# Performance work log

Hardware: AMD Instinct MI355X
Metric: run time of the kernel (lower is better)

The kernel has to match this reference:

```python
import jax, jax.numpy as jnp
import numpy as np

B, S, D = 4, 2048, 1024
H = 16
HD = D // H
PF = 4096
EPS = 1e-5


def setup_inputs() -> dict:
    key = jax.random.key(0)
    ks = jax.random.split(key, 16)
    s = 1.0 / np.sqrt(D)
    inp = {
        'src': jax.random.normal(ks[0], (B, S, D), jnp.float32),
        'Wq': jax.random.normal(ks[1], (D, D), jnp.float32) * s,
        'bq': jnp.zeros((D,), jnp.float32),
        'Wk': jax.random.normal(ks[2], (D, D), jnp.float32) * s,
        'bk': jnp.zeros((D,), jnp.float32),
        'Wv': jax.random.normal(ks[3], (D, D), jnp.float32) * s,
        'bv': jnp.zeros((D,), jnp.float32),
        'Wo': jax.random.normal(ks[4], (D, D), jnp.float32) * s,
        'bo': jnp.zeros((D,), jnp.float32),
        'g1': jnp.ones((D,), jnp.float32),
        'b1': jnp.zeros((D,), jnp.float32),
        'W1': jax.random.normal(ks[5], (D, PF), jnp.float32) * s,
        'bf1': jnp.zeros((PF,), jnp.float32),
        'W2': jax.random.normal(ks[6], (PF, D), jnp.float32) * (1.0 / np.sqrt(PF)),
        'bf2': jnp.zeros((D,), jnp.float32),
        'g2': jnp.ones((D,), jnp.float32),
        'b2': jnp.zeros((D,), jnp.float32),
    }
    return inp


def _layer_norm(x, g, b):
    mu = jnp.mean(x, axis=-1, keepdims=True)
    var = jnp.mean(jnp.square(x - mu), axis=-1, keepdims=True)
    return (x - mu) * jax.lax.rsqrt(var + EPS) * g + b


def reference(src, Wq, bq, Wk, bk, Wv, bv, Wo, bo, g1, b1, W1, bf1, W2, bf2, g2, b2):
    scale = 1.0 / np.sqrt(HD)
    # QKV projections -> [B, H, S, HD]
    q = (src @ Wq + bq).reshape(B, S, H, HD).transpose(0, 2, 1, 3)
    k = (src @ Wk + bk).reshape(B, S, H, HD).transpose(0, 2, 1, 3)
    v = (src @ Wv + bv).reshape(B, S, H, HD).transpose(0, 2, 1, 3)
    # attention scores [B, H, S, S]
    attn = jax.nn.softmax(jnp.einsum('bhqd,bhkd->bhqk', q, k) * scale, axis=-1)
    x = jnp.einsum('bhqk,bhkd->bhqd', attn, v)
    x = x.transpose(0, 2, 1, 3).reshape(B, S, D)
    attn_out = x @ Wo + bo
    # residual + LN (dropout is identity at p=0)
    src1 = _layer_norm(src + attn_out, g1, b1)
    # positionwise FFN: Linear -> Dropout -> ReLU -> Linear
    ff = jax.nn.relu(src1 @ W1 + bf1) @ W2 + bf2
    return _layer_norm(src1 + ff, g2, b2)
```

## Files before the change

### kernel.cpp

```cpp
#include <hip/hip_runtime.h>

#define BB 4
#define SS 2048
#define DD 1024
#define HH 16
#define PFF 4096
#define MR 8192

typedef unsigned short u16;
typedef __attribute__((ext_vector_type(8))) short s16x8;
typedef __attribute__((ext_vector_type(4))) float f32x4v;
typedef __attribute__((ext_vector_type(16))) float f32x16;
typedef __attribute__((ext_vector_type(4))) unsigned short u16x4;
typedef __attribute__((ext_vector_type(8))) unsigned short u16x8;

__device__ inline u16 f2bf(float f) {
  union { float f; unsigned u; } v; v.f = f;
  unsigned r = v.u + 0x7FFFu + ((v.u >> 16) & 1u);
  return (u16)(r >> 16);
}

__device__ inline float bf2f(u16 x) {
  union { unsigned u; float f; } v;
  v.u = ((unsigned)x) << 16;
  return v.f;
}

__device__ inline unsigned cvtpk_bf16(float lo, float hi) {
  unsigned r;
  asm("v_cvt_pk_bf16_f32 %0, %1, %2" : "=v"(r) : "v"(lo), "v"(hi));
  return r;
}

__device__ inline void gload16(const void* g, void* l) {
  __builtin_amdgcn_global_load_lds(
      (const __attribute__((address_space(1))) void*)g,
      (__attribute__((address_space(3))) void*)l, 16, 0, 0);
}

__device__ inline f32x4v MFMA(s16x8 a, s16x8 b, f32x4v c) {
  return __builtin_amdgcn_mfma_f32_16x16x32_bf16(a, b, c, 0, 0, 0);
}
__device__ inline f32x16 MFMA32(s16x8 a, s16x8 b, f32x16 c) {
  return __builtin_amdgcn_mfma_f32_32x32x16_bf16(a, b, c, 0, 0, 0);
}

#define RAWBAR()                          \
  do {                                    \
    asm volatile("" ::: "memory");        \
    __builtin_amdgcn_s_barrier();         \
    asm volatile("" ::: "memory");        \
  } while (0)
#define WAITVM(N) asm volatile("s_waitcnt vmcnt(" #N ")" ::: "memory")

__device__ inline s16x8 ldfrag(const u16* base, int row, int colByte) {
  return *(const s16x8*)((const char*)base + row * 128 + (colByte ^ ((row & 7) << 4)));
}

template <int RELU, int OUTBF, int SCQ, int VT>
__global__ __launch_bounds__(512, 1) void gemm256(
    const u16* __restrict__ A, const u16* __restrict__ Bt,
    const float* __restrict__ bias, float* __restrict__ Cf,
    u16* __restrict__ Cb, u16* __restrict__ Vt, int M, int N, int K,
    int ntx) {
  constexpr int BUF = 16384;
  __shared__ __align__(128) u16 lds[3 * BUF];
  const int t = threadIdx.x;
  const int lane = t & 63, w = t >> 6;
  const int wr = w >> 2, wc = w & 3;
  const int g = lane >> 4, q = lane & 15;

  const int cpx = gridDim.x >> 3;
  const int wg = (blockIdx.x & 7) * cpx + (blockIdx.x >> 3);
  const int row0 = (wg / ntx) * 256, col0 = (wg % ntx) * 256;

  f32x4v acc[8][4];
#pragma unroll
  for (int m = 0; m < 8; ++m)
#pragma unroll
    for (int n = 0; n < 4; ++n) acc[m][n] = (f32x4v){0.f, 0.f, 0.f, 0.f};

  const int sr0 = t >> 2, sc0 = (t & 3) * 8;
  const u16* Ag0 = A + (size_t)(row0 + sr0) * K + sc0;
  const u16* Ag1 = A + (size_t)(row0 + sr0 + 128) * K + sc0;
  const u16* Bg0 = Bt + (size_t)(col0 + sr0) * K + sc0;
  const u16* Bg1 = Bt + (size_t)(col0 + sr0 + 128) * K + sc0;
  const int wud = (t & ~63) * 8;

#define STAGE_A(kt, buf)                                          \
  do {                                                            \
    u16* ab_ = &lds[(buf) * BUF];                                 \
    gload16(Ag0 + (kt) * 32, ab_ + wud);                          \
    gload16(Ag1 + (kt) * 32, ab_ + 4096 + wud);                   \
  } while (0)
#define STAGE_B(kt, buf)                                          \
  do {                                                            \
    u16* bb_ = &lds[(buf) * BUF + 8192];                          \
    gload16(Bg0 + (kt) * 32, bb_ + wud);                          \
    gload16(Bg1 + (kt) * 32, bb_ + 4096 + wud);                   \
  } while (0)

  const int NT = K / 32;
  STAGE_A(0, 0); STAGE_B(0, 0);
  STAGE_A(1, 1); STAGE_B(1, 1);
  WAITVM(4);
  RAWBAR();

  int cur = 0, nxt = 2;
  for (int kt = 0; kt < NT; ++kt) {
    const u16* ab = &lds[cur * BUF];
    const u16* bb = ab + 8192;
    const bool pf = (kt + 2 < NT);
    if (pf) STAGE_A(kt + 2, nxt);
    s16x8 bf_[4], af_[4];
#pragma unroll
    for (int n = 0; n < 4; ++n)
      bf_[n] = *(const s16x8*)&bb[(wc * 64 + n * 16 + q) * 32 + g * 8];
#pragma unroll
    for (int m = 0; m < 4; ++m)
      af_[m] = *(const s16x8*)&ab[(wr * 128 + m * 16 + q) * 32 + g * 8];
    RAWBAR();
    __builtin_amdgcn_s_setprio(1);
#pragma unroll
    for (int m = 0; m < 4; ++m)
#pragma unroll
      for (int n = 0; n < 4; ++n) acc[m][n] = MFMA(af_[m], bf_[n], acc[m][n]);
    __builtin_amdgcn_s_setprio(0);
    RAWBAR();
    if (pf) STAGE_B(kt + 2, nxt);
#pragma unroll
    for (int m = 0; m < 4; ++m)
      af_[m] = *(const s16x8*)&ab[(wr * 128 + (m + 4) * 16 + q) * 32 + g * 8];
    RAWBAR();
    __builtin_amdgcn_s_setprio(1);
#pragma unroll
    for (int m = 0; m < 4; ++m)
#pragma unroll
      for (int n = 0; n < 4; ++n)
        acc[m + 4][n] = MFMA(af_[m], bf_[n], acc[m + 4][n]);
    __builtin_amdgcn_s_setprio(0);
    if (kt + 1 < NT) {
      if (pf) WAITVM(4);
      else WAITVM(0);
    }
    RAWBAR();
    cur = (cur == 2) ? 0 : cur + 1;
    nxt = (nxt == 2) ? 0 : nxt + 1;
  }
#undef STAGE_A
#undef STAGE_B

#pragma unroll
  for (int n = 0; n < 4; ++n) {
    const int col = col0 + wc * 64 + 16 * n + q;
    const float bv = bias ? bias[col] : 0.f;
#pragma unroll
    for (int m = 0; m < 8; ++m) {
      const int row = row0 + wr * 128 + 16 * m + 4 * g;
      if (VT && col >= 2048) {
        const int hd = col - 2048;
        u16x4 o;
#pragma unroll
        for (int r = 0; r < 4; ++r) o[r] = f2bf(acc[m][n][r] + bv);
        *(u16x4*)&Vt[((size_t)((row >> 11) * 16 + (hd >> 6)) * 64 +
                      (hd & 63)) * SS + (row & 2047)] = o;
      } else {
#pragma unroll
        for (int r = 0; r < 4; ++r) {
          float v = acc[m][n][r] + bv;
          if (RELU) v = fmaxf(v, 0.f);
          if (SCQ && col < DD) v *= 0.18033688011112042f;
          if (OUTBF) Cb[(size_t)(row + r) * N + col] = f2bf(v);
          else Cf[(size_t)(row + r) * N + col] = v;
        }
      }
    }
  }
}

template <int RELU>
__global__ __launch_bounds__(256, 3) void gemm128(
    const u16* __restrict__ A, const u16* __restrict__ Bt,
    const float* __restrict__ bias, float* __restrict__ Cf,
    int M, int N, int K, int ntx) {
  constexpr int BUF = 8192;
  __shared__ __align__(128) u16 lds[3 * BUF];
  const int t = threadIdx.x;
  const int lane = t & 63, w = t >> 6;
  const int wr = w >> 1, wc = w & 1;
  const int g = lane >> 4, q = lane & 15;

  const int cpx = gridDim.x >> 3;
  const int wg = (blockIdx.x & 7) * cpx + (blockIdx.x >> 3);
  const int row0 = (wg / ntx) * 128, col0 = (wg % ntx) * 128;

  f32x4v acc[4][4];
#pragma unroll
  for (int m = 0; m < 4; ++m)
#pragma unroll
    for (int n = 0; n < 4; ++n) acc[m][n] = (f32x4v){0.f, 0.f, 0.f, 0.f};

  const int sr0 = t >> 2, sc0 = (t & 3) * 8;
  const u16* Ag0 = A + (size_t)(row0 + sr0) * K + sc0;
  const u16* Ag1 = A + (size_t)(row0 + sr0 + 64) * K + sc0;
  const u16* Bg0 = Bt + (size_t)(col0 + sr0) * K + sc0;
  const u16* Bg1 = Bt + (size_t)(col0 + sr0 + 64) * K + sc0;
  const int wud = (t & ~63) * 8;

#define STAGE_A(kt, buf)                                          \
  do {                                                            \
    u16* ab_ = &lds[(buf) * BUF];                                 \
    gload16(Ag0 + (kt) * 32, ab_ + wud);                          \
    gload16(Ag1 + (kt) * 32, ab_ + 2048 + wud);                   \
  } while (0)
#define STAGE_B(kt, buf)                                          \
  do {                                                            \
    u16* bb_ = &lds[(buf) * BUF + 4096];                          \
    gload16(Bg0 + (kt) * 32, bb_ + wud);                          \
    gload16(Bg1 + (kt) * 32, bb_ + 2048 + wud);                   \
  } while (0)

  const int NT = K / 32;
  STAGE_A(0, 0); STAGE_B(0, 0);
  STAGE_A(1, 1); STAGE_B(1, 1);
  WAITVM(4);
  RAWBAR();

  int cur = 0, nxt = 2;
  for (int kt = 0; kt < NT; ++kt) {
    const u16* ab = &lds[cur * BUF];
    const u16* bb = ab + 4096;
    const bool pf = (kt + 2 < NT);
    if (pf) STAGE_A(kt + 2, nxt);
    s16x8 bf_[4], af_[2];
#pragma unroll
    for (int n = 0; n < 4; ++n)
      bf_[n] = *(const s16x8*)&bb[(wc * 64 + n * 16 + q) * 32 + g * 8];
#pragma unroll
    for (int m = 0; m < 2; ++m)
      af_[m] = *(const s16x8*)&ab[(wr * 64 + m * 16 + q) * 32 + g * 8];
    RAWBAR();
    __builtin_amdgcn_s_setprio(1);
#pragma unroll
    for (int m = 0; m < 2; ++m)
#pragma unroll
      for (int n = 0; n < 4; ++n) acc[m][n] = MFMA(af_[m], bf_[n], acc[m][n]);
    __builtin_amdgcn_s_setprio(0);
    RAWBAR();
    if (pf) STAGE_B(kt + 2, nxt);
#pragma unroll
    for (int m = 0; m < 2; ++m)
      af_[m] = *(const s16x8*)&ab[(wr * 64 + (m + 2) * 16 + q) * 32 + g * 8];
    RAWBAR();
    __builtin_amdgcn_s_setprio(1);
#pragma unroll
    for (int m = 0; m < 2; ++m)
#pragma unroll
      for (int n = 0; n < 4; ++n)
        acc[m + 2][n] = MFMA(af_[m], bf_[n], acc[m + 2][n]);
    __builtin_amdgcn_s_setprio(0);
    if (kt + 1 < NT) {
      if (pf) WAITVM(4);
      else WAITVM(0);
    }
    RAWBAR();
    cur = (cur == 2) ? 0 : cur + 1;
    nxt = (nxt == 2) ? 0 : nxt + 1;
  }
#undef STAGE_A
#undef STAGE_B

#pragma unroll
  for (int n = 0; n < 4; ++n) {
    const int col = col0 + wc * 64 + 16 * n + q;
    const float bv = bias ? bias[col] : 0.f;
#pragma unroll
    for (int m = 0; m < 4; ++m) {
      const int row = row0 + wr * 64 + 16 * m + 4 * g;
#pragma unroll
      for (int r = 0; r < 4; ++r) {
        float v = acc[m][n][r] + bv;
        if (RELU) v = fmaxf(v, 0.f);
        Cf[(size_t)(row + r) * N + col] = v;
      }
    }
  }
}

__global__ __launch_bounds__(256, 4) void attn_mfma(
    const u16* __restrict__ qkv, const u16* __restrict__ vt,
    u16* __restrict__ xb) {
  __shared__ __align__(128) u16 lds[16384];

  const int t = threadIdx.x;
  const int w = t >> 6, lane = t & 63;
  const int q = lane & 31, hi = lane >> 5;
  const int qg = w >> 1;
  const int kg = w & 1;

  const int flat = blockIdx.x;
  const int xcd = flat & 7;
  const int j = flat >> 3;
  const int bh = xcd * 8 + (j & 7);
  const int qb = j >> 3;
  const int b = bh >> 4, h = bh & 15;
  const int q0 = qb * 64;
  const int qcol = h * 64, kcol = DD + h * 64;

  const int r0 = t >> 3;
  const int sc = ((t & 7) ^ (r0 & 7)) * 8;
  const int ldst = (t & ~63) * 16;

  const u16* ks0 = qkv + (size_t)(b * SS + r0) * 3072 + kcol + sc;
  const u16* ks1 = ks0 + (size_t)32 * 3072;
  const u16* vs0 = vt + (size_t)(bh * 64 + r0) * SS + sc;
  const u16* vs1 = vs0 + (size_t)32 * SS;

  {
    const u16* Qsrc = qkv + (size_t)(b * SS + q0 + r0) * 3072 + qcol + sc;
    gload16(Qsrc, (char*)lds + ldst);
    gload16(Qsrc + (size_t)32 * 3072, (char*)lds + 4096 + ldst);
  }
  WAITVM(0);
  RAWBAR();
  s16x8 qf[4];
  {
    const u16* Qw = lds + qg * 2048;
#pragma unroll
    for (int s = 0; s < 4; ++s) qf[s] = ldfrag(Qw, q, 32 * s + 16 * hi);
  }
  asm volatile("s_waitcnt lgkmcnt(0)" ::: "memory");
  __builtin_amdgcn_sched_barrier(0);
  RAWBAR();

#define STAGE(B)                                              \
  do {                                                        \
    gload16(ks0, (char*)lds + (B) + ldst);                    \
    gload16(ks1, (char*)lds + (B) + 4096 + ldst);             \
    gload16(vs0, (char*)lds + (B) + 8192 + ldst);             \
    gload16(vs1, (char*)lds + (B) + 12288 + ldst);            \
    ks0 += (size_t)64 * 3072; ks1 += (size_t)64 * 3072;       \
    vs0 += 64; vs1 += 64;                                     \
  } while (0)

  s16x8 onesv;
#pragma unroll
  for (int i = 0; i < 8; ++i) onesv[i] = (short)0x3F80;

  f32x16 zf;
#pragma unroll
  for (int i = 0; i < 16; ++i) zf[i] = 0.f;

  f32x16 oac0, oac1, lacc;
#pragma unroll
  for (int i = 0; i < 16; ++i) { oac0[i] = 0.f; oac1[i] = 0.f; lacc[i] = 0.f; }

  auto compute = [&](const int B) {
    const u16* Kc = lds + B / 2;
    const u16* Vc = Kc + 4096;

    __builtin_amdgcn_s_setprio(1);
    s16x8 k0 = ldfrag(Kc, kg * 32 + q, 16 * hi);
    f32x16 sa = MFMA32(k0, qf[0], zf);
#pragma unroll
    for (int s = 1; s < 4; ++s) {
      s16x8 ks = ldfrag(Kc, kg * 32 + q, 32 * s + 16 * hi);
      sa = MFMA32(ks, qf[s], sa);
    }
    __builtin_amdgcn_s_setprio(0);

#pragma unroll
    for (int i = 0; i < 16; ++i) sa[i] = exp2f(sa[i]);

    __builtin_amdgcn_s_setprio(1);
#pragma unroll
    for (int sp = 0; sp < 2; ++sp) {
      const int rb = 8 * sp;
      unsigned x0 = cvtpk_bf16(sa[rb + 0], sa[rb + 1]);
      unsigned x1 = cvtpk_bf16(sa[rb + 2], sa[rb + 3]);
      unsigned y0 = cvtpk_bf16(sa[rb + 4], sa[rb + 5]);
      unsigned y1 = cvtpk_bf16(sa[rb + 6], sa[rb + 7]);
      asm("v_permlane32_swap_b32 %0, %1" : "+v"(x0), "+v"(y0));
      asm("v_permlane32_swap_b32 %0, %1" : "+v"(x1), "+v"(y1));
      union { unsigned u[4]; s16x8 v; } pfv;
      pfv.u[0] = x0; pfv.u[1] = x1; pfv.u[2] = y0; pfv.u[3] = y1;
      s16x8 v0 = ldfrag(Vc, q, kg * 64 + 32 * sp + 16 * hi);
      s16x8 v1 = ldfrag(Vc, 32 + q, kg * 64 + 32 * sp + 16 * hi);
      oac0 = MFMA32(v0, pfv.v, oac0);
      oac1 = MFMA32(v1, pfv.v, oac1);
      lacc = MFMA32(onesv, pfv.v, lacc);
    }
    __builtin_amdgcn_s_setprio(0);
  };

  STAGE(0);
  WAITVM(0);
  RAWBAR();
  for (int i = 0; i < 15; ++i) {
    STAGE(16384);
    compute(0);
    WAITVM(0);
    RAWBAR();
    STAGE(0);
    compute(16384);
    WAITVM(0);
    RAWBAR();
  }
  STAGE(16384);
  compute(0);
  WAITVM(0);
  RAWBAR();
  compute(16384);
#undef STAGE

  __syncthreads();
  float* red = (float*)lds;
  if (kg == 1) {
    float* myr = red + (qg * 64 + lane) * 33;
#pragma unroll
    for (int i = 0; i < 16; ++i) { myr[i] = oac0[i]; myr[16 + i] = oac1[i]; }
    myr[32] = lacc[0];
  }
  __syncthreads();
  if (kg == 0) {
    const float* pr = red + (qg * 64 + lane) * 33;
#pragma unroll
    for (int i = 0; i < 16; ++i) { oac0[i] += pr[i]; oac1[i] += pr[16 + i]; }
    const float inv = 1.f / (lacc[0] + pr[32]);
    const size_t row = (size_t)(b * SS + q0 + qg * 32 + q);
    u16* orow = xb + row * DD + qcol;
#pragma unroll
    for (int rr = 0; rr < 4; ++rr) {
      uint2 pw0, pw1;
      pw0.x = cvtpk_bf16(oac0[4 * rr] * inv, oac0[4 * rr + 1] * inv);
      pw0.y = cvtpk_bf16(oac0[4 * rr + 2] * inv, oac0[4 * rr + 3] * inv);
      pw1.x = cvtpk_bf16(oac1[4 * rr] * inv, oac1[4 * rr + 1] * inv);
      pw1.y = cvtpk_bf16(oac1[4 * rr + 2] * inv, oac1[4 * rr + 3] * inv);
      *(uint2*)(orow + 8 * rr + 4 * hi) = pw0;
      *(uint2*)(orow + 32 + 8 * rr + 4 * hi) = pw1;
    }
  }
}

__global__ __launch_bounds__(256) void cvt_bf16(const float* __restrict__ x,
                                                u16* __restrict__ y, int n4) {
  int i = blockIdx.x * 256 + threadIdx.x;
  if (i < n4) {
    float4 v = ((const float4*)x)[i];
    u16x4 o;
    o[0] = f2bf(v.x); o[1] = f2bf(v.y); o[2] = f2bf(v.z); o[3] = f2bf(v.w);
    ((u16x4*)y)[i] = o;
  }
}

__global__ __launch_bounds__(256) void transpose_w(const float* __restrict__ W,
                                                   u16* __restrict__ Wt,
                                                   int K, int N) {
  __shared__ float T[32][33];
  const int n0 = blockIdx.x * 32, k0 = blockIdx.y * 32;
  const int t = threadIdx.x;
  const int r = t >> 3, c = (t & 7) * 4;
  float4 v = *(const float4*)&W[(size_t)(k0 + r) * N + n0 + c];
  T[r][c] = v.x; T[r][c + 1] = v.y; T[r][c + 2] = v.z; T[r][c + 3] = v.w;
  __syncthreads();
  const int a = t >> 3, b0 = (t & 7) * 4;
  u16x4 o;
#pragma unroll
  for (int j = 0; j < 4; ++j) o[j] = f2bf(T[b0 + j][a]);
  *(u16x4*)&Wt[(size_t)(n0 + a) * K + k0 + b0] = o;
}

__global__ __launch_bounds__(256) void concat3(const float* __restrict__ a,
                                               const float* __restrict__ b,
                                               const float* __restrict__ c,
                                               float* __restrict__ o) {
  int i = blockIdx.x * 256 + threadIdx.x;
  if (i < 3072)
    o[i] = i < 1024 ? a[i] : (i < 2048 ? b[i - 1024] : c[i - 2048]);
}

template <int WB, int WF, int XBF>
__global__ __launch_bounds__(256) void ln_res(
    const float* __restrict__ Xf, const u16* __restrict__ Xb,
    const float* __restrict__ R, const float* __restrict__ g,
    const float* __restrict__ b, float* __restrict__ Y,
    u16* __restrict__ Yb) {
  const int row = blockIdx.x;
  const int t = threadIdx.x;
  const size_t off = (size_t)row * DD + t * 4;

  float v0, v1, v2, v3;
  if (XBF) {
    u16x4 x4 = *(const u16x4*)&Xb[off];
    v0 = bf2f(x4[0]); v1 = bf2f(x4[1]); v2 = bf2f(x4[2]); v3 = bf2f(x4[3]);
  } else {
    float4 x4 = *(const float4*)&Xf[off];
    v0 = x4.x; v1 = x4.y; v2 = x4.z; v3 = x4.w;
  }
  float4 r4 = *(const float4*)&R[off];
  v0 += r4.x; v1 += r4.y; v2 += r4.z; v3 += r4.w;

  float s1 = v0 + v1 + v2 + v3;
  float s2 = v0 * v0 + v1 * v1 + v2 * v2 + v3 * v3;
#pragma unroll
  for (int o = 1; o < 64; o <<= 1) {
    s1 += __shfl_xor(s1, o);
    s2 += __shfl_xor(s2, o);
  }
  __shared__ float red1[4], red2[4];
  if ((t & 63) == 0) {
    red1[t >> 6] = s1;
    red2[t >> 6] = s2;
  }
  __syncthreads();
  s1 = red1[0] + red1[1] + red1[2] + red1[3];
  s2 = red2[0] + red2[1] + red2[2] + red2[3];

  const float mu = s1 * (1.f / DD);
  const float var = s2 * (1.f / DD) - mu * mu;
  const float rs = rsqrtf(var + 1e-5f);

  float4 g4 = *(const float4*)&g[t * 4];
  float4 b4 = *(const float4*)&b[t * 4];
  float4 y;
  y.x = (v0 - mu) * rs * g4.x + b4.x;
  y.y = (v1 - mu) * rs * g4.y + b4.y;
  y.z = (v2 - mu) * rs * g4.z + b4.z;
  y.w = (v3 - mu) * rs * g4.w + b4.w;
  if (WF) *(float4*)&Y[off] = y;
  if (WB) {
    u16x4 o;
    o[0] = f2bf(y.x); o[1] = f2bf(y.y); o[2] = f2bf(y.z); o[3] = f2bf(y.w);
    *(u16x4*)&Yb[off] = o;
  }
}

extern "C" void kernel_launch(void* const* d_in, const int* in_sizes, int n_in,
                              void* d_out, int out_size, void* d_ws,
                              size_t ws_size, hipStream_t stream) {
  const float* src = (const float*)d_in[0];
  const float* Wq  = (const float*)d_in[1];
  const float* bq  = (const float*)d_in[2];
  const float* Wk  = (const float*)d_in[3];
  const float* bk  = (const float*)d_in[4];
  const float* Wv  = (const float*)d_in[5];
  const float* bv  = (const float*)d_in[6];
  const float* Wo  = (const float*)d_in[7];
  const float* bo  = (const float*)d_in[8];
  const float* g1  = (const float*)d_in[9];
  const float* b1  = (const float*)d_in[10];
  const float* W1  = (const float*)d_in[11];
  const float* bf1 = (const float*)d_in[12];
  const float* W2  = (const float*)d_in[13];
  const float* bf2 = (const float*)d_in[14];
  const float* g2  = (const float*)d_in[15];
  const float* b2  = (const float*)d_in[16];

  char* W = (char*)d_ws;
  u16*   wqkvT = (u16*)  (W + 0);
  u16*   woT   = (u16*)  (W + 6291456);
  u16*   w1T   = (u16*)  (W + 8388608);
  u16*   w2T   = (u16*)  (W + 16777216);
  float* bqkv  = (float*)(W + 25165824);
  u16*   srcb  = (u16*)  (W + 25178112);
  u16*   qkv   = (u16*)  (W + 41955328);
  u16*   vt    = (u16*)  (W + 92286976);
  u16*   xb    = (u16*)  (W + 109064192);
  float* pb    = (float*)(W + 125841408);
  u16*   s1bb  = (u16*)  (W + 109064192);
  u16*   f1b   = (u16*)  (W + 41955328);
  float* f2b   = (float*)(W + 125841408);

  dim3 blk(256);

  cvt_bf16<<<8192, blk, 0, stream>>>(src, srcb, MR * DD / 4);
  transpose_w<<<dim3(32, 32), blk, 0, stream>>>(Wq, wqkvT, DD, DD);
  transpose_w<<<dim3(32, 32), blk, 0, stream>>>(Wk, wqkvT + (size_t)1024 * 1024, DD, DD);
  transpose_w<<<dim3(32, 32), blk, 0, stream>>>(Wv, wqkvT + (size_t)2048 * 1024, DD, DD);
  transpose_w<<<dim3(32, 32), blk, 0, stream>>>(Wo, woT, DD, DD);
  transpose_w<<<dim3(128, 32), blk, 0, stream>>>(W1, w1T, DD, PFF);
  transpose_w<<<dim3(32, 128), blk, 0, stream>>>(W2, w2T, PFF, DD);
  concat3<<<12, blk, 0, stream>>>(bq, bk, bv, bqkv);

  gemm256<0, 1, 1, 1><<<384, 512, 0, stream>>>(
      srcb, wqkvT, bqkv, nullptr, qkv, vt, MR, 3072, DD, 12);
  attn_mfma<<<2048, blk, 0, stream>>>(qkv, vt, xb);
  gemm128<0><<<512, blk, 0, stream>>>(xb, woT, bo, pb, MR, DD, DD, 8);
  ln_res<1, 0, 0><<<MR, blk, 0, stream>>>(src, nullptr, pb, g1, b1, nullptr,
                                          s1bb);
  gemm256<1, 1, 0, 0><<<512, 512, 0, stream>>>(
      s1bb, w1T, bf1, nullptr, f1b, nullptr, MR, PFF, DD, 16);
  gemm128<0><<<512, blk, 0, stream>>>(f1b, w2T, bf2, f2b, MR, DD, PFF, 8);
  ln_res<0, 1, 1><<<MR, blk, 0, stream>>>(nullptr, s1bb, f2b, g2, b2,
                                          (float*)d_out, nullptr);
}
```

Before: 441.2 us.

## Merge preprocessing kernels into one launch and raise attention occupancy bound

Replaces the source bf16 conversion, six weight-transpose launches and the bias concat with a single prep_all kernel that dispatches on block index. This removes seven kernel launches and the gaps between those small dependent-free kernels. It also raises the attention kernel's launch_bounds min-blocks hint from 4 to 5, which may cap register use and cause spills.

```diff
diff --git a/kernel.cpp b/kernel.cpp
--- a/kernel.cpp
+++ b/kernel.cpp
@@ -287,7 +287,7 @@
   }
 }
 
-__global__ __launch_bounds__(256, 4) void attn_mfma(
+__global__ __launch_bounds__(256, 5) void attn_mfma(
     const u16* __restrict__ qkv, const u16* __restrict__ vt,
     u16* __restrict__ xb) {
   __shared__ __align__(128) u16 lds[16384];
@@ -442,23 +442,48 @@
   }
 }
 
-__global__ __launch_bounds__(256) void cvt_bf16(const float* __restrict__ x,
-                                                u16* __restrict__ y, int n4) {
-  int i = blockIdx.x * 256 + threadIdx.x;
-  if (i < n4) {
-    float4 v = ((const float4*)x)[i];
+__global__ __launch_bounds__(256) void prep_all(
+    const float* __restrict__ src, u16* __restrict__ srcb,
+    const float* __restrict__ Wq, const float* __restrict__ Wk,
+    const float* __restrict__ Wv, const float* __restrict__ Wo,
+    u16* __restrict__ wqkvT, u16* __restrict__ woT,
+    const float* __restrict__ W1, u16* __restrict__ w1T,
+    const float* __restrict__ W2, u16* __restrict__ w2T,
+    const float* __restrict__ bq, const float* __restrict__ bk,
+    const float* __restrict__ bvv, float* __restrict__ bqkv) {
+  const int id = blockIdx.x;
+  const int t = threadIdx.x;
+  __shared__ float T[32][33];
+
+  if (id < 8192) {
+    int i = id * 256 + t;
+    float4 v = ((const float4*)src)[i];
     u16x4 o;
     o[0] = f2bf(v.x); o[1] = f2bf(v.y); o[2] = f2bf(v.z); o[3] = f2bf(v.w);
-    ((u16x4*)y)[i] = o;
-  }
-}
-
-__global__ __launch_bounds__(256) void transpose_w(const float* __restrict__ W,
-                                                   u16* __restrict__ Wt,
-                                                   int K, int N) {
-  __shared__ float T[32][33];
-  const int n0 = blockIdx.x * 32, k0 = blockIdx.y * 32;
-  const int t = threadIdx.x;
+    ((u16x4*)srcb)[i] = o;
+    return;
+  }
+  const int id2 = id - 8192;
+  if (id2 >= 12288) {
+    int i = (id2 - 12288) * 256 + t;
+    if (i < 3072)
+      bqkv[i] = i < 1024 ? bq[i] : (i < 2048 ? bk[i - 1024] : bvv[i - 2048]);
+    return;
+  }
+  const float* W; u16* Wt; int K, N, bx, by;
+  if (id2 < 4096) {
+    const int which = id2 >> 10, tile = id2 & 1023;
+    W = (which == 0) ? Wq : (which == 1) ? Wk : (which == 2) ? Wv : Wo;
+    Wt = (which == 3) ? woT : wqkvT + (size_t)which * 1024 * 1024;
+    K = 1024; N = 1024; bx = tile & 31; by = tile >> 5;
+  } else if (id2 < 8192) {
+    const int tile = id2 - 4096;
+    W = W1; Wt = w1T; K = 1024; N = 4096; bx = tile & 127; by = tile >> 7;
+  } else {
+    const int tile = id2 - 8192;
+    W = W2; Wt = w2T; K = 4096; N = 1024; bx = tile & 31; by = tile >> 5;
+  }
+  const int n0 = bx * 32, k0 = by * 32;
   const int r = t >> 3, c = (t & 7) * 4;
   float4 v = *(const float4*)&W[(size_t)(k0 + r) * N + n0 + c];
   T[r][c] = v.x; T[r][c + 1] = v.y; T[r][c + 2] = v.z; T[r][c + 3] = v.w;
@@ -466,17 +491,8 @@
   const int a = t >> 3, b0 = (t & 7) * 4;
   u16x4 o;
 #pragma unroll
-  for (int j = 0; j < 4; ++j) o[j] = f2bf(T[b0 + j][a]);
+  for (int jj = 0; jj < 4; ++jj) o[jj] = f2bf(T[b0 + jj][a]);
   *(u16x4*)&Wt[(size_t)(n0 + a) * K + k0 + b0] = o;
-}
-
-__global__ __launch_bounds__(256) void concat3(const float* __restrict__ a,
-                                               const float* __restrict__ b,
-                                               const float* __restrict__ c,
-                                               float* __restrict__ o) {
-  int i = blockIdx.x * 256 + threadIdx.x;
-  if (i < 3072)
-    o[i] = i < 1024 ? a[i] : (i < 2048 ? b[i - 1024] : c[i - 2048]);
 }
 
 template <int WB, int WF, int XBF>
@@ -573,14 +589,8 @@
 
   dim3 blk(256);
 
-  cvt_bf16<<<8192, blk, 0, stream>>>(src, srcb, MR * DD / 4);
-  transpose_w<<<dim3(32, 32), blk, 0, stream>>>(Wq, wqkvT, DD, DD);
-  transpose_w<<<dim3(32, 32), blk, 0, stream>>>(Wk, wqkvT + (size_t)1024 * 1024, DD, DD);
-  transpose_w<<<dim3(32, 32), blk, 0, stream>>>(Wv, wqkvT + (size_t)2048 * 1024, DD, DD);
-  transpose_w<<<dim3(32, 32), blk, 0, stream>>>(Wo, woT, DD, DD);
-  transpose_w<<<dim3(128, 32), blk, 0, stream>>>(W1, w1T, DD, PFF);
-  transpose_w<<<dim3(32, 128), blk, 0, stream>>>(W2, w2T, PFF, DD);
-  concat3<<<12, blk, 0, stream>>>(bq, bk, bv, bqkv);
+  prep_all<<<20492, blk, 0, stream>>>(src, srcb, Wq, Wk, Wv, Wo, wqkvT, woT,
+                                      W1, w1T, W2, w2T, bq, bk, bv, bqkv);
 
   gemm256<0, 1, 1, 1><<<384, 512, 0, stream>>>(
       srcb, wqkvT, bqkv, nullptr, qkv, vt, MR, 3072, DD, 12);
```

Result: slower. 519.3 us (+17.7%).
